# Performance work log

Hardware: AMD Instinct MI355X
Metric: run time of the kernel (lower is better)

## Reference

```python
import jax, jax.numpy as jnp
import numpy as np

N = 8192
IN_DIM = 256
OUT_DIM = 64
ALPHA = 0.2  # LeakyReLU negative slope


def setup_inputs() -> dict:
    key = jax.random.key(0)
    k1, k2, k3 = jax.random.split(key, 3)
    h = jax.random.normal(k1, (N, IN_DIM), dtype=jnp.float32)
    adj = jnp.zeros((N, N), dtype=jnp.bool_)  # accepted by forward but unused (faithful to source)
    # xavier_uniform-ish scale for params
    W = jax.random.normal(k2, (IN_DIM, OUT_DIM), dtype=jnp.float32) * (1.414 * (2.0 / (IN_DIM + OUT_DIM)) ** 0.5)
    a = jax.random.normal(k3, (2 * OUT_DIM, 1), dtype=jnp.float32) * (1.414 * (2.0 / (2 * OUT_DIM + 1)) ** 0.5)
    return {"h": h, "adj": adj, "W": W, "a": a}


def reference(h, adj, W, a):
    # Wh: [N, D]
    Wh = h @ W
    d = Wh.shape[1]
    Wh1 = Wh @ a[:d]   # [N, 1]
    Wh2 = Wh @ a[d:]   # [N, 1]
    # e: [N, N] dense additive attention scores (adj is NOT used in the source)
    e = jax.nn.leaky_relu(Wh1 + Wh2.T, negative_slope=ALPHA)
    attention = jax.nn.softmax(e, axis=1)
    # dropout(p=0.6) is identity in eval mode
    h_prime = attention @ Wh  # [N, D]
    return jax.nn.elu(h_prime)
```

## Files before the change

kernel.cpp:

```cpp
#include <hip/hip_runtime.h>
#include <math.h>

#define NN 8192
#define KDIM 256
#define DD 64
#define NB 4096
#define NBLK 256
#define NTHR 512
#define RPB 32
#define CH 32
#define NCH 256
#define LRALPHA 0.2f

__device__ __forceinline__ unsigned f2k(float f) {
    unsigned u = __float_as_uint(f);
    return u ^ ((u >> 31) ? 0xFFFFFFFFu : 0x80000000u);
}
__device__ __forceinline__ float k2f(unsigned k) {
    return __uint_as_float((k & 0x80000000u) ? (k ^ 0x80000000u) : ~k);
}
__device__ __forceinline__ unsigned bucket_of(unsigned key, unsigned kmin, float scale) {
    unsigned d = key - kmin;
    unsigned b = (unsigned)((float)d * scale);
    return b > (NB - 1) ? (NB - 1) : b;
}

__device__ __forceinline__ void  cstf(float* p, float v) { __hip_atomic_store(p, v, __ATOMIC_RELAXED, __HIP_MEMORY_SCOPE_AGENT); }
__device__ __forceinline__ float cldf(const float* p)    { return __hip_atomic_load((float*)p, __ATOMIC_RELAXED, __HIP_MEMORY_SCOPE_AGENT); }

__device__ __forceinline__ void gridbar(unsigned* flags, unsigned* rel, unsigned phase) {
    asm volatile("s_waitcnt vmcnt(0)" ::: "memory");
    __syncthreads();
    const int t = threadIdx.x;
    if (blockIdx.x == 0) {
        if (t == 0)
            __hip_atomic_store(&flags[0], phase, __ATOMIC_RELAXED, __HIP_MEMORY_SCOPE_AGENT);
        if (t < NBLK) {
            while (__hip_atomic_load(&flags[t], __ATOMIC_RELAXED, __HIP_MEMORY_SCOPE_AGENT) < phase)
                __builtin_amdgcn_s_sleep(1);
        }
        __syncthreads();
        if (t == 0)
            __hip_atomic_store(rel, phase, __ATOMIC_RELAXED, __HIP_MEMORY_SCOPE_AGENT);
    } else {
        if (t == 0) {
            __hip_atomic_store(&flags[blockIdx.x], phase, __ATOMIC_RELAXED, __HIP_MEMORY_SCOPE_AGENT);
            while (__hip_atomic_load(rel, __ATOMIC_RELAXED, __HIP_MEMORY_SCOPE_AGENT) < phase)
                __builtin_amdgcn_s_sleep(1);
        }
        __syncthreads();
    }
}

__global__ __launch_bounds__(NTHR, 2) void k_fused(
    const float* __restrict__ h, const float* __restrict__ W,
    const float* __restrict__ a, float* __restrict__ out,
    float* Wh2g, float* sv, float* wnv, float* wpv, float* sg,
    float* cs_neg, float* cs_pos, float* cs_sn, float* cs_sp,
    float* PN, float* SP, float* PNs, float* SPs,
    int* cnt, unsigned* flags, unsigned* rel)
{
    __shared__ int      ls_bstart[NB + 1];
    __shared__ float    ls_wh1[RPB];
    __shared__ float    ls_wh2[RPB];
    __shared__ unsigned ls_ra[8], ls_rb[8];
    __shared__ int      ls_wsum[8];
    __shared__ float    ls_cs[8][2 * DD];
    __shared__ float    ls_css[16];
    __shared__ float    ls_M2, ls_scale;
    __shared__ unsigned ls_kmin;

    const int t = threadIdx.x, bid = blockIdx.x;
    const int wv = t >> 6, lane = t & 63;
    const int rowBase = bid * RPB;

    float myrow[4];
    {
        const int r0 = rowBase + wv * 4;
        float acc0 = 0.f, acc1 = 0.f, acc2 = 0.f, acc3 = 0.f;
        #pragma unroll 2
        for (int k4 = 0; k4 < KDIM / 4; ++k4) {
            float w0 = W[(4 * k4 + 0) * DD + lane];
            float w1 = W[(4 * k4 + 1) * DD + lane];
            float w2 = W[(4 * k4 + 2) * DD + lane];
            float w3 = W[(4 * k4 + 3) * DD + lane];
            float4 h0 = *(const float4*)(h + (size_t)(r0 + 0) * KDIM + 4 * k4);
            float4 h1 = *(const float4*)(h + (size_t)(r0 + 1) * KDIM + 4 * k4);
            float4 h2 = *(const float4*)(h + (size_t)(r0 + 2) * KDIM + 4 * k4);
            float4 h3 = *(const float4*)(h + (size_t)(r0 + 3) * KDIM + 4 * k4);
            acc0 = fmaf(h0.x, w0, acc0); acc0 = fmaf(h0.y, w1, acc0);
            acc0 = fmaf(h0.z, w2, acc0); acc0 = fmaf(h0.w, w3, acc0);
            acc1 = fmaf(h1.x, w0, acc1); acc1 = fmaf(h1.y, w1, acc1);
            acc1 = fmaf(h1.z, w2, acc1); acc1 = fmaf(h1.w, w3, acc1);
            acc2 = fmaf(h2.x, w0, acc2); acc2 = fmaf(h2.y, w1, acc2);
            acc2 = fmaf(h2.z, w2, acc2); acc2 = fmaf(h2.w, w3, acc2);
            acc3 = fmaf(h3.x, w0, acc3); acc3 = fmaf(h3.y, w1, acc3);
            acc3 = fmaf(h3.z, w2, acc3); acc3 = fmaf(h3.w, w3, acc3);
        }
        myrow[0] = acc0; myrow[1] = acc1; myrow[2] = acc2; myrow[3] = acc3;
        float a1 = a[lane], a2 = a[DD + lane];
        #pragma unroll
        for (int i = 0; i < 4; ++i) {
            float r1 = myrow[i] * a1, r2 = myrow[i] * a2;
            #pragma unroll
            for (int off = 32; off > 0; off >>= 1) {
                r1 += __shfl_xor(r1, off, 64);
                r2 += __shfl_xor(r2, off, 64);
            }
            if (lane == 0) {
                cstf(&Wh2g[r0 + i], r2);
                ls_wh1[wv * 4 + i] = r1;
                ls_wh2[wv * 4 + i] = r2;
            }
        }
    }
    gridbar(flags, rel, 1);

    for (int i = t; i < NB; i += NTHR) ls_bstart[i] = 0;
    float v16[16];
    #pragma unroll
    for (int q = 0; q < 16; ++q)
        v16[q] = cldf(&Wh2g[t + q * NTHR]);
    {
        unsigned lmin = 0xFFFFFFFFu, lmax = 0u;
        #pragma unroll
        for (int q = 0; q < 16; ++q) {
            unsigned k = f2k(v16[q]);
            lmin = min(lmin, k); lmax = max(lmax, k);
        }
        #pragma unroll
        for (int off = 32; off > 0; off >>= 1) {
            lmin = min(lmin, (unsigned)__shfl_xor((int)lmin, off, 64));
            lmax = max(lmax, (unsigned)__shfl_xor((int)lmax, off, 64));
        }
        if (lane == 0) { ls_ra[wv] = lmin; ls_rb[wv] = lmax; }
    }
    __syncthreads();
    if (t == 0) {
        unsigned mn = ls_ra[0], mx = ls_rb[0];
        for (int i = 1; i < 8; ++i) { mn = min(mn, ls_ra[i]); mx = max(mx, ls_rb[i]); }
        ls_kmin = mn;
        ls_scale = (float)NB / ((float)(mx - mn) + 1.0f);
        ls_M2 = k2f(mx);
    }
    __syncthreads();
    const unsigned kmin = ls_kmin;
    const float scale = ls_scale;
    const float M2 = ls_M2;

    #pragma unroll
    for (int q = 0; q < 16; ++q)
        atomicAdd(&ls_bstart[bucket_of(f2k(v16[q]), kmin, scale)], 1);
    __syncthreads();
    {
        int s[8]; int tot = 0;
        #pragma unroll
        for (int j = 0; j < 8; ++j) { s[j] = ls_bstart[8 * t + j]; tot += s[j]; }
        int x = tot;
        #pragma unroll
        for (int off = 1; off < 64; off <<= 1) {
            int y = __shfl_up(x, off, 64);
            if (lane >= off) x += y;
        }
        if (lane == 63) ls_wsum[wv] = x;
        __syncthreads();
        int woff = 0;
        for (int w2 = 0; w2 < wv; ++w2) woff += ls_wsum[w2];
        int acc = woff + x - tot;
        #pragma unroll
        for (int j = 0; j < 8; ++j) { ls_bstart[8 * t + j] = acc; acc += s[j]; }
        if (t == 0) ls_bstart[NB] = NN;
    }
    __syncthreads();
    {
        int posl = 0;
        if (lane < 4) {
            unsigned b = bucket_of(f2k(ls_wh2[wv * 4 + lane]), kmin, scale);
            posl = ls_bstart[b] + atomicAdd(&cnt[b], 1);
        }
        #pragma unroll
        for (int i = 0; i < 4; ++i) {
            int lr = wv * 4 + i;
            float x = ls_wh2[lr];
            int pos = __shfl(posl, i, 64);
            cstf(&sg[(size_t)pos * DD + lane], myrow[i]);
            if (lane == 0) {
                cstf(&sv[pos], x);
                cstf(&wnv[pos], expf(LRALPHA * (x - M2)));
                cstf(&wpv[pos], expf(x - M2));
            }
        }
    }
    gridbar(flags, rel, 2);

    {
        int base = bid * CH + wv * 4;
        float g4[4], wn4[4], wp4[4];
        #pragma unroll
        for (int kk = 0; kk < 4; ++kk) {
            int k = base + kk;
            g4[kk]  = cldf(&sg[(size_t)k * DD + lane]);
            wn4[kk] = cldf(&wnv[k]);
            wp4[kk] = cldf(&wpv[k]);
        }
        float an = 0.f, ap = 0.f, sn = 0.f, sp = 0.f;
        #pragma unroll
        for (int kk = 0; kk < 4; ++kk) {
            an = fmaf(wn4[kk], g4[kk], an); ap = fmaf(wp4[kk], g4[kk], ap);
            sn += wn4[kk]; sp += wp4[kk];
        }
        ls_cs[wv][lane] = an; ls_cs[wv][DD + lane] = ap;
        if (lane == 0) { ls_css[wv] = sn; ls_css[8 + wv] = sp; }
        __syncthreads();
        if (wv == 0) {
            float s = 0.f;
            #pragma unroll
            for (int w2 = 0; w2 < 8; ++w2) s += ls_cs[w2][lane];
            cstf(&cs_neg[bid * DD + lane], s);
            if (lane == 0) { float ss = 0.f; for (int w2 = 0; w2 < 8; ++w2) ss += ls_css[w2]; cstf(&cs_sn[bid], ss); }
        } else if (wv == 1) {
            float s = 0.f;
            #pragma unroll
            for (int w2 = 0; w2 < 8; ++w2) s += ls_cs[w2][DD + lane];
            cstf(&cs_pos[bid * DD + lane], s);
            if (lane == 0) { float ss = 0.f; for (int w2 = 0; w2 < 8; ++w2) ss += ls_css[8 + w2]; cstf(&cs_sp[bid], ss); }
        }
    }
    gridbar(flags, rel, 3);

    if (bid == 0) {
        const int c0 = wv * 32;
        float v[32];
        #pragma unroll
        for (int j = 0; j < 32; ++j) v[j] = cldf(&cs_neg[(c0 + j) * DD + lane]);
        float tot = 0.f;
        #pragma unroll
        for (int j = 0; j < 32; ++j) tot += v[j];
        ls_cs[wv][lane] = tot;
        __syncthreads();
        float acc = 0.f;
        for (int w2 = 0; w2 < wv; ++w2) acc += ls_cs[w2][lane];
        #pragma unroll
        for (int j = 0; j < 32; ++j) { cstf(&PN[(c0 + j) * DD + lane], acc); acc += v[j]; }
        if (wv == 7) cstf(&PN[NCH * DD + lane], acc);
    } else if (bid == 1) {
        const int c0 = wv * 32;
        float v[32];
        #pragma unroll
        for (int j = 0; j < 32; ++j) v[j] = cldf(&cs_pos[(c0 + j) * DD + lane]);
        float tot = 0.f;
        #pragma unroll
        for (int j = 0; j < 32; ++j) tot += v[j];
        ls_cs[wv][lane] = tot;
        __syncthreads();
        float acc = 0.f;
        for (int w2 = wv + 1; w2 < 8; ++w2) acc += ls_cs[w2][lane];
        #pragma unroll
        for (int j = 31; j >= 0; --j) { acc += v[j]; cstf(&SP[(c0 + j) * DD + lane], acc); }
        if (wv == 7) cstf(&SP[NCH * DD + lane], 0.f);
    } else if (bid == 2) {
        if (wv == 0) {
            float s[4];
            #pragma unroll
            for (int j = 0; j < 4; ++j) s[j] = cldf(&cs_sn[4 * lane + j]);
            float tot = s[0] + s[1] + s[2] + s[3];
            float x = tot;
            #pragma unroll
            for (int off = 1; off < 64; off <<= 1) {
                float y = __shfl_up(x, off, 64);
                if (lane >= off) x += y;
            }
            float acc = x - tot;
            #pragma unroll
            for (int j = 0; j < 4; ++j) { cstf(&PNs[4 * lane + j], acc); acc += s[j]; }
            if (lane == 63) cstf(&PNs[NCH], acc);
        } else if (wv == 1) {
            float s[4];
            #pragma unroll
            for (int j = 0; j < 4; ++j) s[j] = cldf(&cs_sp[4 * lane + j]);
            float tot = s[0] + s[1] + s[2] + s[3];
            float x = tot;
            #pragma unroll
            for (int off = 1; off < 64; off <<= 1) {
                float y = __shfl_down(x, off, 64);
                if (lane < 64 - off) x += y;
            }
            float acc = x - tot;
            #pragma unroll
            for (int j = 3; j >= 0; --j) { acc += s[j]; cstf(&SPs[4 * lane + j], acc); }
            if (lane == 63) cstf(&SPs[NCH], 0.f);
        }
    }
    gridbar(flags, rel, 4);

    int c0f4[4], c1e4[4];
    #pragma unroll
    for (int i = 0; i < 4; ++i) {
        float tt = -ls_wh1[wv * 4 + i];
        unsigned kt = f2k(tt);
        int p0 = 0, p1 = 0;
        if (kt >= kmin) {
            unsigned b = bucket_of(kt, kmin, scale);
            p0 = ls_bstart[b]; p1 = ls_bstart[b + 1];
        }
        c0f4[i] = p0 >> 5;
        c1e4[i] = (p1 + 31) >> 5;
    }
    float pn4[4], sp4[4], pns4[4], sps4[4];
    #pragma unroll
    for (int i = 0; i < 4; ++i) {
        pn4[i]  = cldf(&PN[c0f4[i] * DD + lane]);
        sp4[i]  = cldf(&SP[c1e4[i] * DD + lane]);
        pns4[i] = cldf(&PNs[c0f4[i]]);
        sps4[i] = cldf(&SPs[c1e4[i]]);
    }
    #pragma unroll
    for (int i = 0; i < 4; ++i) {
        int row = rowBase + wv * 4 + i;
        float w1 = ls_wh1[wv * 4 + i];
        float z = w1 + M2;
        float m = (z >= 0.f) ? z : LRALPHA * z;
        float c1 = expf(z - m);
        float c2 = expf(LRALPHA * z - m);
        float tt = -w1;
        float nn_ = pn4[i], dn_ = pns4[i];
        float np_ = sp4[i], dp_ = sps4[i];
        for (int base2 = c0f4[i] * CH; base2 < c1e4[i] * CH; base2 += 8) {
            float sv8[8], wn8[8], wp8[8], g8[8];
            #pragma unroll
            for (int jj = 0; jj < 8; ++jj) {
                int k = base2 + jj;
                sv8[jj] = cldf(&sv[k]);
                wn8[jj] = cldf(&wnv[k]);
                wp8[jj] = cldf(&wpv[k]);
                g8[jj]  = cldf(&sg[(size_t)k * DD + lane]);
            }
            #pragma unroll
            for (int jj = 0; jj < 8; ++jj) {
                if (sv8[jj] <= tt) { nn_ = fmaf(wn8[jj], g8[jj], nn_); dn_ += wn8[jj]; }
                else               { np_ = fmaf(wp8[jj], g8[jj], np_); dp_ += wp8[jj]; }
            }
        }
        float num = c2 * nn_ + c1 * np_;
        float den = c2 * dn_ + c1 * dp_;
        float r = num / den;
        out[(size_t)row * DD + lane] = (r > 0.f) ? r : expm1f(r);
    }
}

extern "C" void kernel_launch(void* const* d_in, const int* in_sizes, int n_in,
                              void* d_out, int out_size, void* d_ws, size_t ws_size,
                              hipStream_t stream)
{
    const float* h = (const float*)d_in[0];
    const float* W = (const float*)d_in[2];
    const float* a = (const float*)d_in[3];
    float* out = (float*)d_out;
    float* ws = (float*)d_ws;

    float* Wh2g   = ws;
    float* sv     = Wh2g + NN;
    float* wnv    = sv + NN;
    float* wpv    = wnv + NN;
    float* sg     = wpv + NN;
    float* cs_neg = sg + (size_t)NN * DD;
    float* cs_pos = cs_neg + NCH * DD;
    float* cs_sn  = cs_pos + NCH * DD;
    float* cs_sp  = cs_sn + NCH;
    float* PN     = cs_sp + NCH;
    float* SP     = PN + (NCH + 1) * DD;
    float* PNs    = SP + (NCH + 1) * DD;
    float* SPs    = PNs + 320;
    unsigned* flags = (unsigned*)(SPs + 320);
    unsigned* rel   = flags + NBLK;
    int*   cnt    = (int*)(rel + 256);

    hipMemsetAsync(flags, 0, (NBLK + 256 + NB) * sizeof(unsigned), stream);
    k_fused<<<NBLK, NTHR, 0, stream>>>(h, W, a, out,
        Wh2g, sv, wnv, wpv, sg,
        cs_neg, cs_pos, cs_sn, cs_sp,
        PN, SP, PNs, SPs,
        cnt, flags, rel);
}
```

Baseline: 92.83 us.

## Precompute per-element prefix/suffix sums to shrink boundary scan to one bucket

Adds a new phase that expands the per-chunk prefix (negative) and suffix (positive) weighted sums into per-element prefix arrays, behind an extra grid barrier. The final phase then starts from the exact bucket start and end positions and only scans the elements inside the threshold bucket, instead of whole 32-element chunks. Per-element sort key, negative weight and positive weight are packed into one 16-byte record loaded with 64-bit atomics. The cost is an extra grid-wide barrier, a serial 32-step per-block expansion, and writing about 4 MB of new prefix arrays.

```diff
diff --git a/kernel.cpp b/kernel.cpp
--- a/kernel.cpp
+++ b/kernel.cpp
@@ -27,6 +27,15 @@
 
 __device__ __forceinline__ void  cstf(float* p, float v) { __hip_atomic_store(p, v, __ATOMIC_RELAXED, __HIP_MEMORY_SCOPE_AGENT); }
 __device__ __forceinline__ float cldf(const float* p)    { return __hip_atomic_load((float*)p, __ATOMIC_RELAXED, __HIP_MEMORY_SCOPE_AGENT); }
+__device__ __forceinline__ void cstf2(float* p, float x, float y) {
+    union { unsigned long long u; float f[2]; } c; c.f[0] = x; c.f[1] = y;
+    __hip_atomic_store((unsigned long long*)p, c.u, __ATOMIC_RELAXED, __HIP_MEMORY_SCOPE_AGENT);
+}
+__device__ __forceinline__ float2 cldf2(const float* p) {
+    union { unsigned long long u; float2 f; } c;
+    c.u = __hip_atomic_load((const unsigned long long*)p, __ATOMIC_RELAXED, __HIP_MEMORY_SCOPE_AGENT);
+    return c.f;
+}
 
 __device__ __forceinline__ void gridbar(unsigned* flags, unsigned* rel, unsigned phase) {
     asm volatile("s_waitcnt vmcnt(0)" ::: "memory");
@@ -55,9 +64,10 @@
 __global__ __launch_bounds__(NTHR, 2) void k_fused(
     const float* __restrict__ h, const float* __restrict__ W,
     const float* __restrict__ a, float* __restrict__ out,
-    float* Wh2g, float* sv, float* wnv, float* wpv, float* sg,
+    float* Wh2g, float* svp, float* sg,
     float* cs_neg, float* cs_pos, float* cs_sn, float* cs_sp,
     float* PN, float* SP, float* PNs, float* SPs,
+    float* PNe, float* SPe, float* PNse, float* SPse,
     int* cnt, unsigned* flags, unsigned* rel)
 {
     __shared__ int      ls_bstart[NB + 1];
@@ -67,6 +77,8 @@
     __shared__ int      ls_wsum[8];
     __shared__ float    ls_cs[8][2 * DD];
     __shared__ float    ls_css[16];
+    __shared__ float    ls_g[CH][DD];
+    __shared__ float    ls_wn[CH], ls_wp[CH];
     __shared__ float    ls_M2, ls_scale;
     __shared__ unsigned ls_kmin;
 
@@ -185,9 +197,8 @@
             int pos = __shfl(posl, i, 64);
             cstf(&sg[(size_t)pos * DD + lane], myrow[i]);
             if (lane == 0) {
-                cstf(&sv[pos], x);
-                cstf(&wnv[pos], expf(LRALPHA * (x - M2)));
-                cstf(&wpv[pos], expf(x - M2));
+                cstf2(&svp[4 * pos + 0], x, expf(LRALPHA * (x - M2)));
+                cstf2(&svp[4 * pos + 2], expf(x - M2), 0.f);
             }
         }
     }
@@ -195,19 +206,22 @@
 
     {
         int base = bid * CH + wv * 4;
-        float g4[4], wn4[4], wp4[4];
+        float g4[4]; float2 q01[4], q23[4];
         #pragma unroll
         for (int kk = 0; kk < 4; ++kk) {
             int k = base + kk;
             g4[kk]  = cldf(&sg[(size_t)k * DD + lane]);
-            wn4[kk] = cldf(&wnv[k]);
-            wp4[kk] = cldf(&wpv[k]);
+            q01[kk] = cldf2(&svp[4 * k + 0]);
+            q23[kk] = cldf2(&svp[4 * k + 2]);
         }
         float an = 0.f, ap = 0.f, sn = 0.f, sp = 0.f;
         #pragma unroll
         for (int kk = 0; kk < 4; ++kk) {
-            an = fmaf(wn4[kk], g4[kk], an); ap = fmaf(wp4[kk], g4[kk], ap);
-            sn += wn4[kk]; sp += wp4[kk];
+            float wn = q01[kk].y, wp = q23[kk].x;
+            an = fmaf(wn, g4[kk], an); ap = fmaf(wp, g4[kk], ap);
+            sn += wn; sp += wp;
+            ls_g[wv * 4 + kk][lane] = g4[kk];
+            if (lane == 0) { ls_wn[wv * 4 + kk] = wn; ls_wp[wv * 4 + kk] = wp; }
         }
         ls_cs[wv][lane] = an; ls_cs[wv][DD + lane] = ap;
         if (lane == 0) { ls_css[wv] = sn; ls_css[8 + wv] = sp; }
@@ -293,7 +307,38 @@
     }
     gridbar(flags, rel, 4);
 
-    int c0f4[4], c1e4[4];
+    if (wv == 0) {
+        float accn  = cldf(&PN[bid * DD + lane]);
+        float accns = cldf(&PNs[bid]);
+        for (int k = 0; k < CH; ++k) {
+            int e = bid * CH + k;
+            cstf(&PNe[(size_t)e * DD + lane], accn);
+            if (lane == 0) cstf(&PNse[e], accns);
+            float wn = ls_wn[k], g = ls_g[k][lane];
+            accn = fmaf(wn, g, accn); accns += wn;
+        }
+        if (bid == NBLK - 1) {
+            cstf(&PNe[(size_t)NN * DD + lane], accn);
+            if (lane == 0) cstf(&PNse[NN], accns);
+        }
+    } else if (wv == 1) {
+        float accp  = cldf(&SP[(bid + 1) * DD + lane]);
+        float accps = cldf(&SPs[bid + 1]);
+        for (int k = CH - 1; k >= 0; --k) {
+            int e = bid * CH + k;
+            float wp = ls_wp[k], g = ls_g[k][lane];
+            accp = fmaf(wp, g, accp); accps += wp;
+            cstf(&SPe[(size_t)e * DD + lane], accp);
+            if (lane == 0) cstf(&SPse[e], accps);
+        }
+        if (bid == NBLK - 1) {
+            cstf(&SPe[(size_t)NN * DD + lane], 0.f);
+            if (lane == 0) cstf(&SPse[NN], 0.f);
+        }
+    }
+    gridbar(flags, rel, 5);
+
+    int p0a[4], p1a[4];
     #pragma unroll
     for (int i = 0; i < 4; ++i) {
         float tt = -ls_wh1[wv * 4 + i];
@@ -303,16 +348,15 @@
             unsigned b = bucket_of(kt, kmin, scale);
             p0 = ls_bstart[b]; p1 = ls_bstart[b + 1];
         }
-        c0f4[i] = p0 >> 5;
-        c1e4[i] = (p1 + 31) >> 5;
+        p0a[i] = p0; p1a[i] = p1;
     }
     float pn4[4], sp4[4], pns4[4], sps4[4];
     #pragma unroll
     for (int i = 0; i < 4; ++i) {
-        pn4[i]  = cldf(&PN[c0f4[i] * DD + lane]);
-        sp4[i]  = cldf(&SP[c1e4[i] * DD + lane]);
-        pns4[i] = cldf(&PNs[c0f4[i]]);
-        sps4[i] = cldf(&SPs[c1e4[i]]);
+        pn4[i]  = cldf(&PNe[(size_t)p0a[i] * DD + lane]);
+        sp4[i]  = cldf(&SPe[(size_t)p1a[i] * DD + lane]);
+        pns4[i] = cldf(&PNse[p0a[i]]);
+        sps4[i] = cldf(&SPse[p1a[i]]);
     }
     #pragma unroll
     for (int i = 0; i < 4; ++i) {
@@ -325,20 +369,23 @@
         float tt = -w1;
         float nn_ = pn4[i], dn_ = pns4[i];
         float np_ = sp4[i], dp_ = sps4[i];
-        for (int base2 = c0f4[i] * CH; base2 < c1e4[i] * CH; base2 += 8) {
-            float sv8[8], wn8[8], wp8[8], g8[8];
-            #pragma unroll
-            for (int jj = 0; jj < 8; ++jj) {
-                int k = base2 + jj;
-                sv8[jj] = cldf(&sv[k]);
-                wn8[jj] = cldf(&wnv[k]);
-                wp8[jj] = cldf(&wpv[k]);
-                g8[jj]  = cldf(&sg[(size_t)k * DD + lane]);
-            }
-            #pragma unroll
-            for (int jj = 0; jj < 8; ++jj) {
-                if (sv8[jj] <= tt) { nn_ = fmaf(wn8[jj], g8[jj], nn_); dn_ += wn8[jj]; }
-                else               { np_ = fmaf(wp8[jj], g8[jj], np_); dp_ += wp8[jj]; }
+        int p0 = p0a[i], p1 = p1a[i];
+        for (int k0 = p0; k0 < p1; k0 += 4) {
+            float2 q01[4], q23[4]; float g4[4];
+            #pragma unroll
+            for (int j = 0; j < 4; ++j) {
+                int k = (k0 + j < p1) ? (k0 + j) : (p1 - 1);
+                q01[j] = cldf2(&svp[4 * k + 0]);
+                q23[j] = cldf2(&svp[4 * k + 2]);
+                g4[j]  = cldf(&sg[(size_t)k * DD + lane]);
+            }
+            #pragma unroll
+            for (int j = 0; j < 4; ++j) {
+                if (k0 + j < p1) {
+                    float svv = q01[j].x, wn = q01[j].y, wp = q23[j].x, g = g4[j];
+                    if (svv <= tt) { nn_ = fmaf(wn, g, nn_); dn_ += wn; }
+                    else           { np_ = fmaf(wp, g, np_); dp_ += wp; }
+                }
             }
         }
         float num = c2 * nn_ + c1 * np_;
@@ -359,10 +406,8 @@
     float* ws = (float*)d_ws;
 
     float* Wh2g   = ws;
-    float* sv     = Wh2g + NN;
-    float* wnv    = sv + NN;
-    float* wpv    = wnv + NN;
-    float* sg     = wpv + NN;
+    float* svp    = Wh2g + NN;
+    float* sg     = svp + 4 * NN;
     float* cs_neg = sg + (size_t)NN * DD;
     float* cs_pos = cs_neg + NCH * DD;
     float* cs_sn  = cs_pos + NCH * DD;
@@ -371,14 +416,19 @@
     float* SP     = PN + (NCH + 1) * DD;
     float* PNs    = SP + (NCH + 1) * DD;
     float* SPs    = PNs + 320;
-    unsigned* flags = (unsigned*)(SPs + 320);
+    float* PNe    = SPs + 320;
+    float* SPe    = PNe + (size_t)(NN + 1) * DD;
+    float* PNse   = SPe + (size_t)(NN + 1) * DD;
+    float* SPse   = PNse + (NN + 64);
+    unsigned* flags = (unsigned*)(SPse + (NN + 64));
     unsigned* rel   = flags + NBLK;
     int*   cnt    = (int*)(rel + 256);
 
     hipMemsetAsync(flags, 0, (NBLK + 256 + NB) * sizeof(unsigned), stream);
     k_fused<<<NBLK, NTHR, 0, stream>>>(h, W, a, out,
-        Wh2g, sv, wnv, wpv, sg,
+        Wh2g, svp, sg,
         cs_neg, cs_pos, cs_sn, cs_sp,
         PN, SP, PNs, SPs,
+        PNe, SPe, PNse, SPse,
         cnt, flags, rel);
 }
```

Measured after the change: 108.6 us. 16.9% more time.

## Shrink chunk size to 8 and use flat all-to-all grid barrier

Applied to the files above, without the earlier changes.

Chunk size drops from 32 to 8 rows, giving 1024 chunks. This narrows each row's boundary scan over partially covered chunks, at the cost of larger serial prefix-scan work in blocks 0–2. The grid barrier becomes a flat scheme in which every block polls all flags, removing the master-release round trip but adding polling traffic. The Wh2 gather now uses 64-bit contiguous loads per thread instead of strided scalar loads.

```diff
diff --git a/kernel.cpp b/kernel.cpp
--- a/kernel.cpp
+++ b/kernel.cpp
@@ -8,8 +8,8 @@
 #define NBLK 256
 #define NTHR 512
 #define RPB 32
-#define CH 32
-#define NCH 256
+#define CH 8
+#define NCH 1024
 #define LRALPHA 0.2f
 
 __device__ __forceinline__ unsigned f2k(float f) {
@@ -27,29 +27,23 @@
 
 __device__ __forceinline__ void  cstf(float* p, float v) { __hip_atomic_store(p, v, __ATOMIC_RELAXED, __HIP_MEMORY_SCOPE_AGENT); }
 __device__ __forceinline__ float cldf(const float* p)    { return __hip_atomic_load((float*)p, __ATOMIC_RELAXED, __HIP_MEMORY_SCOPE_AGENT); }
-
-__device__ __forceinline__ void gridbar(unsigned* flags, unsigned* rel, unsigned phase) {
+__device__ __forceinline__ float2 cldf2(const float* p) {
+    union { unsigned long long u; float2 f; } c;
+    c.u = __hip_atomic_load((const unsigned long long*)p, __ATOMIC_RELAXED, __HIP_MEMORY_SCOPE_AGENT);
+    return c.f;
+}
+
+__device__ __forceinline__ void gridbar(unsigned* flags, unsigned phase) {
     asm volatile("s_waitcnt vmcnt(0)" ::: "memory");
     __syncthreads();
     const int t = threadIdx.x;
-    if (blockIdx.x == 0) {
-        if (t == 0)
-            __hip_atomic_store(&flags[0], phase, __ATOMIC_RELAXED, __HIP_MEMORY_SCOPE_AGENT);
-        if (t < NBLK) {
-            while (__hip_atomic_load(&flags[t], __ATOMIC_RELAXED, __HIP_MEMORY_SCOPE_AGENT) < phase)
-                __builtin_amdgcn_s_sleep(1);
-        }
-        __syncthreads();
-        if (t == 0)
-            __hip_atomic_store(rel, phase, __ATOMIC_RELAXED, __HIP_MEMORY_SCOPE_AGENT);
-    } else {
-        if (t == 0) {
-            __hip_atomic_store(&flags[blockIdx.x], phase, __ATOMIC_RELAXED, __HIP_MEMORY_SCOPE_AGENT);
-            while (__hip_atomic_load(rel, __ATOMIC_RELAXED, __HIP_MEMORY_SCOPE_AGENT) < phase)
-                __builtin_amdgcn_s_sleep(1);
-        }
-        __syncthreads();
-    }
+    if (t == 0)
+        __hip_atomic_store(&flags[blockIdx.x], phase, __ATOMIC_RELAXED, __HIP_MEMORY_SCOPE_AGENT);
+    if (t < NBLK) {
+        while (__hip_atomic_load(&flags[t], __ATOMIC_RELAXED, __HIP_MEMORY_SCOPE_AGENT) < phase)
+            __builtin_amdgcn_s_sleep(2);
+    }
+    __syncthreads();
 }
 
 __global__ __launch_bounds__(NTHR, 2) void k_fused(
@@ -58,7 +52,7 @@
     float* Wh2g, float* sv, float* wnv, float* wpv, float* sg,
     float* cs_neg, float* cs_pos, float* cs_sn, float* cs_sp,
     float* PN, float* SP, float* PNs, float* SPs,
-    int* cnt, unsigned* flags, unsigned* rel)
+    int* cnt, unsigned* flags)
 {
     __shared__ int      ls_bstart[NB + 1];
     __shared__ float    ls_wh1[RPB];
@@ -114,13 +108,15 @@
             }
         }
     }
-    gridbar(flags, rel, 1);
+    gridbar(flags, 1);
 
     for (int i = t; i < NB; i += NTHR) ls_bstart[i] = 0;
     float v16[16];
     #pragma unroll
-    for (int q = 0; q < 16; ++q)
-        v16[q] = cldf(&Wh2g[t + q * NTHR]);
+    for (int q = 0; q < 8; ++q) {
+        float2 p2 = cldf2(&Wh2g[t * 16 + 2 * q]);
+        v16[2 * q] = p2.x; v16[2 * q + 1] = p2.y;
+    }
     {
         unsigned lmin = 0xFFFFFFFFu, lmax = 0u;
         #pragma unroll
@@ -191,10 +187,10 @@
             }
         }
     }
-    gridbar(flags, rel, 2);
-
-    {
-        int base = bid * CH + wv * 4;
+    gridbar(flags, 2);
+
+    {
+        int base = rowBase + wv * 4;
         float g4[4], wn4[4], wp4[4];
         #pragma unroll
         for (int kk = 0; kk < 4; ++kk) {
@@ -212,58 +208,59 @@
         ls_cs[wv][lane] = an; ls_cs[wv][DD + lane] = ap;
         if (lane == 0) { ls_css[wv] = sn; ls_css[8 + wv] = sp; }
         __syncthreads();
-        if (wv == 0) {
-            float s = 0.f;
-            #pragma unroll
-            for (int w2 = 0; w2 < 8; ++w2) s += ls_cs[w2][lane];
-            cstf(&cs_neg[bid * DD + lane], s);
-            if (lane == 0) { float ss = 0.f; for (int w2 = 0; w2 < 8; ++w2) ss += ls_css[w2]; cstf(&cs_sn[bid], ss); }
-        } else if (wv == 1) {
-            float s = 0.f;
-            #pragma unroll
-            for (int w2 = 0; w2 < 8; ++w2) s += ls_cs[w2][DD + lane];
-            cstf(&cs_pos[bid * DD + lane], s);
-            if (lane == 0) { float ss = 0.f; for (int w2 = 0; w2 < 8; ++w2) ss += ls_css[8 + w2]; cstf(&cs_sp[bid], ss); }
-        }
-    }
-    gridbar(flags, rel, 3);
+        if (wv < 4) {
+            int c = bid * 4 + wv;
+            float s = ls_cs[2 * wv][lane] + ls_cs[2 * wv + 1][lane];
+            cstf(&cs_neg[(size_t)c * DD + lane], s);
+            if (lane == 0) cstf(&cs_sn[c], ls_css[2 * wv] + ls_css[2 * wv + 1]);
+        } else {
+            int cw = wv - 4;
+            int c = bid * 4 + cw;
+            float s = ls_cs[2 * cw][DD + lane] + ls_cs[2 * cw + 1][DD + lane];
+            cstf(&cs_pos[(size_t)c * DD + lane], s);
+            if (lane == 0) cstf(&cs_sp[c], ls_css[8 + 2 * cw] + ls_css[8 + 2 * cw + 1]);
+        }
+    }
+    gridbar(flags, 3);
 
     if (bid == 0) {
-        const int c0 = wv * 32;
-        float v[32];
-        #pragma unroll
-        for (int j = 0; j < 32; ++j) v[j] = cldf(&cs_neg[(c0 + j) * DD + lane]);
+        const int c0 = wv * 128;
+        float v[128];
+        #pragma unroll
+        for (int j = 0; j < 128; ++j) v[j] = cldf(&cs_neg[(size_t)(c0 + j) * DD + lane]);
         float tot = 0.f;
         #pragma unroll
-        for (int j = 0; j < 32; ++j) tot += v[j];
+        for (int j = 0; j < 128; ++j) tot += v[j];
         ls_cs[wv][lane] = tot;
         __syncthreads();
         float acc = 0.f;
         for (int w2 = 0; w2 < wv; ++w2) acc += ls_cs[w2][lane];
         #pragma unroll
-        for (int j = 0; j < 32; ++j) { cstf(&PN[(c0 + j) * DD + lane], acc); acc += v[j]; }
-        if (wv == 7) cstf(&PN[NCH * DD + lane], acc);
+        for (int j = 0; j < 128; ++j) { cstf(&PN[(size_t)(c0 + j) * DD + lane], acc); acc += v[j]; }
+        if (wv == 7) cstf(&PN[(size_t)NCH * DD + lane], acc);
     } else if (bid == 1) {
-        const int c0 = wv * 32;
-        float v[32];
-        #pragma unroll
-        for (int j = 0; j < 32; ++j) v[j] = cldf(&cs_pos[(c0 + j) * DD + lane]);
+        const int c0 = wv * 128;
+        float v[128];
+        #pragma unroll
+        for (int j = 0; j < 128; ++j) v[j] = cldf(&cs_pos[(size_t)(c0 + j) * DD + lane]);
         float tot = 0.f;
         #pragma unroll
-        for (int j = 0; j < 32; ++j) tot += v[j];
+        for (int j = 0; j < 128; ++j) tot += v[j];
         ls_cs[wv][lane] = tot;
         __syncthreads();
         float acc = 0.f;
         for (int w2 = wv + 1; w2 < 8; ++w2) acc += ls_cs[w2][lane];
         #pragma unroll
-        for (int j = 31; j >= 0; --j) { acc += v[j]; cstf(&SP[(c0 + j) * DD + lane], acc); }
-        if (wv == 7) cstf(&SP[NCH * DD + lane], 0.f);
+        for (int j = 127; j >= 0; --j) { acc += v[j]; cstf(&SP[(size_t)(c0 + j) * DD + lane], acc); }
+        if (wv == 7) cstf(&SP[(size_t)NCH * DD + lane], 0.f);
     } else if (bid == 2) {
         if (wv == 0) {
-            float s[4];
-            #pragma unroll
-            for (int j = 0; j < 4; ++j) s[j] = cldf(&cs_sn[4 * lane + j]);
-            float tot = s[0] + s[1] + s[2] + s[3];
+            float s[16];
+            #pragma unroll
+            for (int j = 0; j < 16; ++j) s[j] = cldf(&cs_sn[16 * lane + j]);
+            float tot = 0.f;
+            #pragma unroll
+            for (int j = 0; j < 16; ++j) tot += s[j];
             float x = tot;
             #pragma unroll
             for (int off = 1; off < 64; off <<= 1) {
@@ -272,13 +269,15 @@
             }
             float acc = x - tot;
             #pragma unroll
-            for (int j = 0; j < 4; ++j) { cstf(&PNs[4 * lane + j], acc); acc += s[j]; }
+            for (int j = 0; j < 16; ++j) { cstf(&PNs[16 * lane + j], acc); acc += s[j]; }
             if (lane == 63) cstf(&PNs[NCH], acc);
         } else if (wv == 1) {
-            float s[4];
-            #pragma unroll
-            for (int j = 0; j < 4; ++j) s[j] = cldf(&cs_sp[4 * lane + j]);
-            float tot = s[0] + s[1] + s[2] + s[3];
+            float s[16];
+            #pragma unroll
+            for (int j = 0; j < 16; ++j) s[j] = cldf(&cs_sp[16 * lane + j]);
+            float tot = 0.f;
+            #pragma unroll
+            for (int j = 0; j < 16; ++j) tot += s[j];
             float x = tot;
             #pragma unroll
             for (int off = 1; off < 64; off <<= 1) {
@@ -287,11 +286,11 @@
             }
             float acc = x - tot;
             #pragma unroll
-            for (int j = 3; j >= 0; --j) { acc += s[j]; cstf(&SPs[4 * lane + j], acc); }
+            for (int j = 15; j >= 0; --j) { acc += s[j]; cstf(&SPs[16 * lane + j], acc); }
             if (lane == 63) cstf(&SPs[NCH], 0.f);
         }
     }
-    gridbar(flags, rel, 4);
+    gridbar(flags, 4);
 
     int c0f4[4], c1e4[4];
     #pragma unroll
@@ -303,14 +302,14 @@
             unsigned b = bucket_of(kt, kmin, scale);
             p0 = ls_bstart[b]; p1 = ls_bstart[b + 1];
         }
-        c0f4[i] = p0 >> 5;
-        c1e4[i] = (p1 + 31) >> 5;
+        c0f4[i] = p0 >> 3;
+        c1e4[i] = (p1 + 7) >> 3;
     }
     float pn4[4], sp4[4], pns4[4], sps4[4];
     #pragma unroll
     for (int i = 0; i < 4; ++i) {
-        pn4[i]  = cldf(&PN[c0f4[i] * DD + lane]);
-        sp4[i]  = cldf(&SP[c1e4[i] * DD + lane]);
+        pn4[i]  = cldf(&PN[(size_t)c0f4[i] * DD + lane]);
+        sp4[i]  = cldf(&SP[(size_t)c1e4[i] * DD + lane]);
         pns4[i] = cldf(&PNs[c0f4[i]]);
         sps4[i] = cldf(&SPs[c1e4[i]]);
     }
@@ -364,21 +363,20 @@
     float* wpv    = wnv + NN;
     float* sg     = wpv + NN;
     float* cs_neg = sg + (size_t)NN * DD;
-    float* cs_pos = cs_neg + NCH * DD;
-    float* cs_sn  = cs_pos + NCH * DD;
-    float* cs_sp  = cs_sn + NCH;
-    float* PN     = cs_sp + NCH;
-    float* SP     = PN + (NCH + 1) * DD;
-    float* PNs    = SP + (NCH + 1) * DD;
-    float* SPs    = PNs + 320;
-    unsigned* flags = (unsigned*)(SPs + 320);
-    unsigned* rel   = flags + NBLK;
-    int*   cnt    = (int*)(rel + 256);
-
-    hipMemsetAsync(flags, 0, (NBLK + 256 + NB) * sizeof(unsigned), stream);
+    float* cs_pos = cs_neg + (size_t)NCH * DD;
+    float* cs_sn  = cs_pos + (size_t)NCH * DD;
+    float* cs_sp  = cs_sn + 1088;
+    float* PN     = cs_sp + 1088;
+    float* SP     = PN + (size_t)(NCH + 1) * DD;
+    float* PNs    = SP + (size_t)(NCH + 1) * DD;
+    float* SPs    = PNs + 1088;
+    unsigned* flags = (unsigned*)(SPs + 1088);
+    int*   cnt    = (int*)(flags + NBLK);
+
+    hipMemsetAsync(flags, 0, (NBLK + NB) * sizeof(unsigned), stream);
     k_fused<<<NBLK, NTHR, 0, stream>>>(h, W, a, out,
         Wh2g, sv, wnv, wpv, sg,
         cs_neg, cs_pos, cs_sn, cs_sp,
         PN, SP, PNs, SPs,
-        cnt, flags, rel);
-}
+        cnt, flags);
+}
```

After: 143.1 us. +54.1%, slower.
